# Performance work log

Measured on AMD Instinct MI355X. Metric: run time of the kernel, lower is better.

Reference implementation:

```python
import jax, jax.numpy as jnp
import numpy as np

IMG = 224
PS = 2
C_IN = 3
EMBED = 768
BATCH = 256
SLICES = IMG // 2            # 112
L = 2 * (SLICES // PS)       # 112 levels
K = IMG * PS                 # 448 gathered (a,b) pairs per level
D_IN = K * C_IN              # 1344


def _build_levels(n=IMG, slices=SLICES, ps=PS):
    """Replicates LUnraveling index construction (natural order; set() in the
    original only permutes within a level, which is equivalent up to a fixed
    permutation of weight columns for random init)."""
    a_list, b_list = [], []
    ar = np.arange(n)
    for i in range(slices // ps):
        cols = range(i * ps, (i + 1) * ps)
        # 'up' level: pairs (j, col) for j in range(n), concatenated over ps cols
        a_list.append(np.concatenate([ar for _ in cols]))
        b_list.append(np.concatenate([np.full(n, c) for c in cols]))
        # 'right' level: pairs (n - slices + col, j) for j in range(n)
        a_list.append(np.concatenate([np.full(n, n - slices + c) for c in cols]))
        b_list.append(np.concatenate([ar for _ in cols]))
    return (np.stack(a_list).astype(np.int32), np.stack(b_list).astype(np.int32))


def setup_inputs() -> dict:
    key = jax.random.key(0)
    k1, k2, k3 = jax.random.split(key, 3)
    x = jax.random.normal(k1, (BATCH, C_IN, IMG, IMG), dtype=jnp.float32)
    W = jax.random.normal(k2, (EMBED, D_IN), dtype=jnp.float32) * (1.0 / np.sqrt(D_IN))
    b = jax.random.normal(k3, (EMBED,), dtype=jnp.float32) * 0.01
    a_np, b_np = _build_levels()
    return {"x": x, "W": W, "b": b,
            "a_idx": jnp.asarray(a_np), "b_idx": jnp.asarray(b_np)}


def reference(x, W, b, a_idx, b_idx):
    B = x.shape[0]
    # gather: x[:, :, a, b] with (L,K) index arrays -> (B, C, L, K)
    g = x[:, :, a_idx, b_idx]
    # per-level flatten(1) in torch flattens (C, K) C-major -> (B, L, C*K)
    g = jnp.transpose(g, (0, 2, 1, 3)).reshape(B, L, C_IN * K)
    # shared linear projection per level token
    tokens = jnp.einsum('bld,ed->ble', g, W) + b
    return tokens  # (B, L, EMBED); norm is Identity (norm_layer=None)
```

## Files before the change

### kernel.cpp

```cpp
#include <hip/hip_runtime.h>
#include <stdint.h>


#define IMG   224
#define NLEV  112
#define CIN   3
#define DIN   1344
#define EMB   768
#define BATCH 256
#define MTOT  28672
#define NT    21

#define BM    128
#define BN    128
#define BK    64
#define LDP   72

#define AS1 __attribute__((address_space(1)))
#define AS3 __attribute__((address_space(3)))

typedef __attribute__((ext_vector_type(8))) short   short8;
typedef __attribute__((ext_vector_type(4))) float   floatx4;

__device__ __forceinline__ unsigned short f2bf(float f) {
    unsigned u = __float_as_uint(f);
    unsigned r = (u + 0x7fffu + ((u >> 16) & 1u)) >> 16;
    return (unsigned short)r;
}
__device__ __forceinline__ float bf2f(unsigned short s) {
    return __uint_as_float(((unsigned)s) << 16);
}
__device__ __forceinline__ unsigned pack2(float a, float b) {
    return (unsigned)f2bf(a) | ((unsigned)f2bf(b) << 16);
}

__global__ void detect_dtype(const unsigned short* __restrict__ W, int* flag) {
    __shared__ int s;
    if (threadIdx.x == 0) s = 0;
    __syncthreads();
    int bad = 0;
    for (int k = threadIdx.x; k < 4096; k += 256) {
        unsigned v = (unsigned)W[2 * k] & 0x7FFFu;
        if (v >= 0x4000u) bad = 1;
    }
    if (bad) atomicOr(&s, 1);
    __syncthreads();
    if (threadIdx.x == 0) *flag = s;
}

__global__ __launch_bounds__(256)
void pack_all(const void* __restrict__ Xv, const void* __restrict__ Wv,
              const void* __restrict__ Bv,
              unsigned short* __restrict__ Gc, unsigned short* __restrict__ Wb,
              float* __restrict__ Bf, int b0, int chb, int doW)
{
    __shared__ __align__(16) unsigned short lds[IMG * 128];
    __shared__ int sflag;

    const int tid = threadIdx.x;

    {
        if (tid == 0) sflag = 0;
        int bad = 0;
        const unsigned short* Wu = (const unsigned short*)Wv;
        #pragma unroll
        for (int k = tid; k < 512; k += 256) {
            unsigned v = (unsigned)Wu[2 * k] & 0x7FFFu;
            if (v >= 0x4000u) bad = 1;
        }
        __syncthreads();
        if (bad) atomicOr(&sflag, 1);
        __syncthreads();
    }
    const bool F32 = (sflag != 0);

    if (blockIdx.y == 3) {
        if (!doW) return;
        const int total = EMB * DIN / 8;
        for (int idx = blockIdx.x * 256 + tid; idx < total; idx += chb * 256) {
            if (F32) {
                const float4* s = (const float4*)((const float*)Wv + (size_t)idx * 8);
                float4 x0 = s[0], x1 = s[1];
                uint4 o;
                o.x = pack2(x0.x, x0.y); o.y = pack2(x0.z, x0.w);
                o.z = pack2(x1.x, x1.y); o.w = pack2(x1.z, x1.w);
                ((uint4*)Wb)[idx] = o;
            } else {
                ((uint4*)Wb)[idx] = ((const uint4*)Wv)[idx];
            }
        }
        if (blockIdx.x == 0) {
            for (int e = tid; e < EMB; e += 256)
                Bf[e] = F32 ? ((const float*)Bv)[e]
                            : bf2f(((const unsigned short*)Bv)[e]);
        }
        return;
    }

    const int bl = blockIdx.x;
    const int c  = blockIdx.y;
    const size_t plane = ((size_t)(b0 + bl) * CIN + c) * (size_t)(IMG * IMG);
    unsigned short* Grow = Gc + (size_t)bl * NLEV * DIN + (size_t)c * 448;

    if (F32) {
        const float* src = (const float*)Xv + plane + (size_t)NLEV * IMG;
        for (int v = tid; v < 3136; v += 256) {
            const int i  = v / 56;
            const int kk = (v - i * 56) * 8;
            const float4* s = (const float4*)(src + (size_t)v * 8);
            float4 x0 = s[0], x1 = s[1];
            uint4 o;
            o.x = pack2(x0.x, x0.y); o.y = pack2(x0.z, x0.w);
            o.z = pack2(x1.x, x1.y); o.w = pack2(x1.z, x1.w);
            *(uint4*)(Grow + (size_t)(2 * i + 1) * DIN + kk) = o;
        }
    } else {
        const unsigned short* src = (const unsigned short*)Xv + plane + (size_t)NLEV * IMG;
        for (int v = tid; v < 3136; v += 256) {
            const int i  = v / 56;
            const int kk = (v - i * 56) * 8;
            *(uint4*)(Grow + (size_t)(2 * i + 1) * DIN + kk) =
                *(const uint4*)(src + (size_t)v * 8);
        }
    }

    for (int v = tid; v < 3136; v += 256) {
        const int r  = v / 14;
        const int vv = v - r * 14;
        const int key = (r >> 3) & 15;
        uint2 o0, o1;
        if (F32) {
            const float4* s = (const float4*)((const float*)Xv + plane
                              + (size_t)r * IMG + (size_t)vv * 8);
            float4 x0 = s[0], x1 = s[1];
            o0.x = pack2(x0.x, x0.y); o0.y = pack2(x0.z, x0.w);
            o1.x = pack2(x1.x, x1.y); o1.y = pack2(x1.z, x1.w);
        } else {
            const uint2* s = (const uint2*)((const unsigned short*)Xv + plane
                              + (size_t)r * IMG + (size_t)vv * 8);
            o0 = s[0]; o1 = s[1];
        }
        *(uint2*)&lds[r * 128 + ((2 * vv)     ^ key) * 4] = o0;
        *(uint2*)&lds[r * 128 + ((2 * vv + 1) ^ key) * 4] = o1;
    }
    __syncthreads();

    for (int idx = tid; idx < 56 * 56; idx += 256) {
        const int pr   = idx / 56;
        const int j    = idx - pr * 56;
        const int half = j / 28;
        const int r0   = (j - half * 28) * 8;
        const int qb   = pr >> 1;
        const int sh   = (pr & 1) * 2;
        unsigned short h[8];
        #pragma unroll
        for (int m = 0; m < 8; m++) {
            const int r = r0 + m;
            const unsigned v = *(const unsigned*)
                &lds[r * 128 + (qb ^ ((r >> 3) & 15)) * 4 + sh];
            h[m] = half ? (unsigned short)(v >> 16) : (unsigned short)(v & 0xFFFFu);
        }
        uint4 o;
        o.x = (unsigned)h[0] | ((unsigned)h[1] << 16);
        o.y = (unsigned)h[2] | ((unsigned)h[3] << 16);
        o.z = (unsigned)h[4] | ((unsigned)h[5] << 16);
        o.w = (unsigned)h[6] | ((unsigned)h[7] << 16);
        *(uint4*)(Grow + (size_t)(2 * pr) * DIN + half * IMG + r0) = o;
    }
}

__global__ __launch_bounds__(256)
void gemm_packed(const unsigned short* __restrict__ G,
                 const unsigned short* __restrict__ Wb,
                 const float* __restrict__ Bf,
                 float* __restrict__ Out)
{
    __shared__ __align__(16) unsigned short As[2][128 * 64];
    __shared__ __align__(16) unsigned short Bs[2][128 * 64];

    const int tid  = threadIdx.x;
    const int wave = tid >> 6;
    const int lane = tid & 63;

    const int bid = blockIdx.x;
    const int nwg = gridDim.x;
    const int q = nwg >> 3, r = nwg & 7;
    const int xcd = bid & 7, s = bid >> 3;
    const int lid = (xcd < r ? xcd * (q + 1) : r * (q + 1) + (xcd - r) * q) + s;
    const int mT = lid / 6;
    const int nT = lid - mT * 6;
    const int mBase = mT * 128;
    const int nBase = nT * 128;

    const int wm   = wave >> 1, wn = wave & 1;
    const int lrow = lane & 15;
    const int kq   = (lane >> 4) << 3;
    const int swz  = (lrow & 7) << 3;

    floatx4 acc[4][4];
    #pragma unroll
    for (int i = 0; i < 4; i++)
        #pragma unroll
        for (int j = 0; j < 4; j++)
            acc[i][j] = (floatx4){0.f, 0.f, 0.f, 0.f};

    const unsigned short* gaP[4];
    const unsigned short* gbP[4];
    unsigned ldsOff[4];
    #pragma unroll
    for (int i = 0; i < 4; i++) {
        const int idx = (i * 4 + wave) * 64 + lane;
        const int row = idx >> 3, k8 = idx & 7;
        const int jc  = k8 ^ (row & 7);
        gaP[i] = G  + (size_t)(mBase + row) * DIN + jc * 8;
        gbP[i] = Wb + (size_t)(nBase + row) * DIN + jc * 8;
        ldsOff[i] = (unsigned)((i * 4 + wave) * 512);
    }

    #pragma unroll
    for (int i = 0; i < 4; i++) {
        __builtin_amdgcn_global_load_lds((const AS1 void*)(gaP[i]),
                                         (AS3 void*)(&As[0][0] + ldsOff[i]), 16, 0, 0);
        __builtin_amdgcn_global_load_lds((const AS1 void*)(gbP[i]),
                                         (AS3 void*)(&Bs[0][0] + ldsOff[i]), 16, 0, 0);
    }

    int cur = 0;
    for (int t = 0; t < NT; ++t) {
        if (t < NT - 1) {
            const int kt = (t + 1) * 64;
            #pragma unroll
            for (int i = 0; i < 4; i++) {
                __builtin_amdgcn_global_load_lds(
                    (const AS1 void*)(gaP[i] + kt),
                    (AS3 void*)(&As[cur ^ 1][0] + ldsOff[i]), 16, 0, 0);
                __builtin_amdgcn_global_load_lds(
                    (const AS1 void*)(gbP[i] + kt),
                    (AS3 void*)(&Bs[cur ^ 1][0] + ldsOff[i]), 16, 0, 0);
            }
            asm volatile("s_waitcnt vmcnt(8)" ::: "memory");
        } else {
            asm volatile("s_waitcnt vmcnt(0)" ::: "memory");
        }
        __builtin_amdgcn_s_barrier();
        __builtin_amdgcn_sched_barrier(0);

        const unsigned short* Ab = &As[cur][0];
        const unsigned short* Bb = &Bs[cur][0];
        #pragma unroll
        for (int k0 = 0; k0 < 64; k0 += 32) {
            short8 af[4], bfv[4];
            #pragma unroll
            for (int mi = 0; mi < 4; mi++)
                af[mi] = *(const short8*)&Ab[(wm * 64 + mi * 16 + lrow) * 64
                                             + ((k0 + kq) ^ swz)];
            #pragma unroll
            for (int ni = 0; ni < 4; ni++)
                bfv[ni] = *(const short8*)&Bb[(wn * 64 + ni * 16 + lrow) * 64
                                              + ((k0 + kq) ^ swz)];
            __builtin_amdgcn_s_setprio(1);
            #pragma unroll
            for (int mi = 0; mi < 4; mi++)
                #pragma unroll
                for (int ni = 0; ni < 4; ni++)
                    acc[mi][ni] = __builtin_amdgcn_mfma_f32_16x16x32_bf16(
                        af[mi], bfv[ni], acc[mi][ni], 0, 0, 0);
            __builtin_amdgcn_s_setprio(0);
        }
        __builtin_amdgcn_s_barrier();
        __builtin_amdgcn_sched_barrier(0);
        cur ^= 1;
    }

    const int quad = lane >> 4;
    #pragma unroll
    for (int ni = 0; ni < 4; ni++) {
        const int col = nBase + wn * 64 + ni * 16 + lrow;
        const float bv = Bf[col];
        #pragma unroll
        for (int mi = 0; mi < 4; mi++) {
            const int rbase = mBase + wm * 64 + mi * 16 + quad * 4;
            floatx4 a = acc[mi][ni];
            Out[(size_t)(rbase + 0) * EMB + col] = a[0] + bv;
            Out[(size_t)(rbase + 1) * EMB + col] = a[1] + bv;
            Out[(size_t)(rbase + 2) * EMB + col] = a[2] + bv;
            Out[(size_t)(rbase + 3) * EMB + col] = a[3] + bv;
        }
    }
}

template<bool F32>
__global__ __launch_bounds__(256, 2)
void lfreq_fused_gemm(const void* __restrict__ Xv,
                      const void* __restrict__ Wv,
                      const void* __restrict__ Bv,
                      const int* __restrict__ Aidx,
                      const int* __restrict__ Bidx,
                      float* __restrict__ Out,
                      const int* __restrict__ flag)
{
    if (*flag != (F32 ? 1 : 0)) return;

    __shared__ __align__(16) unsigned short As[BM][LDP];
    __shared__ __align__(16) unsigned short Bs[BN][LDP];

    const int tid   = threadIdx.x;
    const int wave  = tid >> 6;
    const int lane  = tid & 63;
    const int mBase = blockIdx.x * BM;
    const int nBase = blockIdx.y * BN;

    const int srow  = tid >> 1;
    const int shalf = tid & 1;
    const int am = mBase + srow;
    const int bb = am / NLEV;
    const int ll = am - bb * NLEV;

    floatx4 acc[4][4];
    #pragma unroll
    for (int i = 0; i < 4; i++)
        #pragma unroll
        for (int jj = 0; jj < 4; jj++)
            acc[i][jj] = (floatx4){0.f, 0.f, 0.f, 0.f};

    const int wm   = wave >> 1;
    const int wn   = wave & 1;
    const int lrow = lane & 15;
    const int kq   = (lane >> 4) << 3;

    for (int kt = 0; kt < DIN; kt += BK) {
        {
            const int koff = kt + shalf * 32;
            uint4* dst = (uint4*)&Bs[srow][shalf * 32];
            if (F32) {
                const float4* g = (const float4*)((const float*)Wv
                                + (size_t)(nBase + srow) * DIN + koff);
                #pragma unroll
                for (int q = 0; q < 4; q++) {
                    float4 v0 = g[2*q], v1 = g[2*q+1];
                    uint4 o;
                    o.x = pack2(v0.x, v0.y); o.y = pack2(v0.z, v0.w);
                    o.z = pack2(v1.x, v1.y); o.w = pack2(v1.z, v1.w);
                    dst[q] = o;
                }
            } else {
                const uint4* g = (const uint4*)((const unsigned short*)Wv
                               + (size_t)(nBase + srow) * DIN + koff);
                #pragma unroll
                for (int q = 0; q < 4; q++) dst[q] = g[q];
            }
        }
        {
            const int d0  = kt + shalf * 32;
            const int c   = (d0 >= 896) ? 2 : (d0 >= 448 ? 1 : 0);
            const int kk0 = d0 - c * 448;
            const int4* ap = (const int4*)(Aidx + ll * 448 + kk0);
            const int4* bp = (const int4*)(Bidx + ll * 448 + kk0);
            unsigned* du = (unsigned*)&As[srow][shalf * 32];
            if (F32) {
                const float* plane = (const float*)Xv
                    + (size_t)bb * (CIN * IMG * IMG) + (size_t)c * (IMG * IMG);
                #pragma unroll
                for (int q = 0; q < 8; q++) {
                    int4 av = ap[q], bv = bp[q];
                    du[2*q+0] = pack2(plane[av.x * IMG + bv.x], plane[av.y * IMG + bv.y]);
                    du[2*q+1] = pack2(plane[av.z * IMG + bv.z], plane[av.w * IMG + bv.w]);
                }
            } else {
                const unsigned short* plane = (const unsigned short*)Xv
                    + (size_t)bb * (CIN * IMG * IMG) + (size_t)c * (IMG * IMG);
                #pragma unroll
                for (int q = 0; q < 8; q++) {
                    int4 av = ap[q], bv = bp[q];
                    unsigned e0 = plane[av.x * IMG + bv.x];
                    unsigned e1 = plane[av.y * IMG + bv.y];
                    unsigned e2 = plane[av.z * IMG + bv.z];
                    unsigned e3 = plane[av.w * IMG + bv.w];
                    du[2*q+0] = e0 | (e1 << 16);
                    du[2*q+1] = e2 | (e3 << 16);
                }
            }
        }
        __syncthreads();

        #pragma unroll
        for (int k0 = 0; k0 < BK; k0 += 32) {
            short8 af[4], bfv[4];
            #pragma unroll
            for (int mi = 0; mi < 4; mi++)
                af[mi] = *(const short8*)&As[wm*64 + mi*16 + lrow][k0 + kq];
            #pragma unroll
            for (int ni = 0; ni < 4; ni++)
                bfv[ni] = *(const short8*)&Bs[wn*64 + ni*16 + lrow][k0 + kq];
            #pragma unroll
            for (int mi = 0; mi < 4; mi++)
                #pragma unroll
                for (int ni = 0; ni < 4; ni++)
                    acc[mi][ni] = __builtin_amdgcn_mfma_f32_16x16x32_bf16(
                        af[mi], bfv[ni], acc[mi][ni], 0, 0, 0);
        }
        __syncthreads();
    }

    const int quad = lane >> 4;
    #pragma unroll
    for (int ni = 0; ni < 4; ni++) {
        const int col = nBase + wn*64 + ni*16 + lrow;
        const float bv = F32 ? ((const float*)Bv)[col]
                             : bf2f(((const unsigned short*)Bv)[col]);
        #pragma unroll
        for (int mi = 0; mi < 4; mi++) {
            const int rbase = mBase + wm*64 + mi*16 + quad*4;
            floatx4 a = acc[mi][ni];
            Out[(size_t)(rbase+0)*EMB + col] = a[0] + bv;
            Out[(size_t)(rbase+1)*EMB + col] = a[1] + bv;
            Out[(size_t)(rbase+2)*EMB + col] = a[2] + bv;
            Out[(size_t)(rbase+3)*EMB + col] = a[3] + bv;
        }
    }
}

extern "C" void kernel_launch(void* const* d_in, const int* in_sizes, int n_in,
                              void* d_out, int out_size, void* d_ws, size_t ws_size,
                              hipStream_t stream) {
    const void* X    = d_in[0];
    const void* Wt   = d_in[1];
    const void* Bias = d_in[2];
    const int*  Ai   = (const int*)d_in[3];
    const int*  Bi   = (const int*)d_in[4];
    float* Out = (float*)d_out;

    char* ws  = (char*)d_ws;
    int* flag = (int*)ws;

    float* Bf          = (float*)(ws + 256);
    unsigned short* Wb = (unsigned short*)(ws + 4096);
    const size_t gOff  = 4096 + (size_t)EMB * DIN * 2;
    unsigned short* Gc = (unsigned short*)(ws + gOff);

    int CHB = 0;
    const int cand[6] = {256, 128, 64, 32, 16, 8};
    for (int t = 0; t < 6; t++) {
        if (gOff + (size_t)cand[t] * NLEV * DIN * 2 <= ws_size) { CHB = cand[t]; break; }
    }

    if (CHB == 0) {
        detect_dtype<<<dim3(1), dim3(256), 0, stream>>>((const unsigned short*)Wt, flag);
        dim3 grid(MTOT / BM, EMB / BN);
        lfreq_fused_gemm<false><<<grid, dim3(256), 0, stream>>>(X, Wt, Bias, Ai, Bi, Out, flag);
        lfreq_fused_gemm<true ><<<grid, dim3(256), 0, stream>>>(X, Wt, Bias, Ai, Bi, Out, flag);
        return;
    }

    for (int b0 = 0; b0 < BATCH; b0 += CHB) {
        dim3 pgrid(CHB, 4);
        pack_all<<<pgrid, dim3(256), 0, stream>>>(X, Wt, Bias, Gc, Wb, Bf,
                                                  b0, CHB, b0 == 0 ? 1 : 0);
        dim3 ggrid(CHB * NLEV / 128 * 6);
        gemm_packed<<<ggrid, dim3(256), 0, stream>>>(Gc, Wb, Bf,
                                                     Out + (size_t)b0 * NLEV * EMB);
    }
}
```

Before: 334.0 us.

## Enlarge GEMM tile to 256x128 and read odd levels directly from input in bf16 mode

The GEMM goes to 512 threads with a 256-row M tile, so each block reuses its loaded W tile across twice as many rows. When the inputs are already bf16, the GEMM now loads the odd 'right' levels straight from the raw image and W straight from the raw weights. This removes the copy passes in the pack kernel for that case. The pack kernel writes the dtype flag for the GEMM to read, and the CHB=8 chunk option is dropped. In the default fp32 path the main effect is the larger tile, which raises register and LDS pressure per block and halves the grid size.

```diff
diff --git a/kernel.cpp b/kernel.cpp
--- a/kernel.cpp
+++ b/kernel.cpp
@@ -10,6 +10,8 @@
 #define BATCH 256
 #define MTOT  28672
 #define NT    21
+#define GBM   256
+#define GBN   128
 
 #define BM    128
 #define BN    128
@@ -52,7 +54,8 @@
 void pack_all(const void* __restrict__ Xv, const void* __restrict__ Wv,
               const void* __restrict__ Bv,
               unsigned short* __restrict__ Gc, unsigned short* __restrict__ Wb,
-              float* __restrict__ Bf, int b0, int chb, int doW)
+              float* __restrict__ Bf, int* __restrict__ flagOut,
+              int b0, int chb, int doW)
 {
     __shared__ __align__(16) unsigned short lds[IMG * 128];
     __shared__ int sflag;
@@ -74,19 +77,20 @@
     }
     const bool F32 = (sflag != 0);
 
+    if (blockIdx.x == 0 && blockIdx.y == 0 && tid == 0)
+        *flagOut = F32 ? 1 : 0;
+
     if (blockIdx.y == 3) {
         if (!doW) return;
-        const int total = EMB * DIN / 8;
-        for (int idx = blockIdx.x * 256 + tid; idx < total; idx += chb * 256) {
-            if (F32) {
+        if (F32) {
+            const int total = EMB * DIN / 8;
+            for (int idx = blockIdx.x * 256 + tid; idx < total; idx += chb * 256) {
                 const float4* s = (const float4*)((const float*)Wv + (size_t)idx * 8);
                 float4 x0 = s[0], x1 = s[1];
                 uint4 o;
                 o.x = pack2(x0.x, x0.y); o.y = pack2(x0.z, x0.w);
                 o.z = pack2(x1.x, x1.y); o.w = pack2(x1.z, x1.w);
                 ((uint4*)Wb)[idx] = o;
-            } else {
-                ((uint4*)Wb)[idx] = ((const uint4*)Wv)[idx];
             }
         }
         if (blockIdx.x == 0) {
@@ -113,14 +117,6 @@
             o.x = pack2(x0.x, x0.y); o.y = pack2(x0.z, x0.w);
             o.z = pack2(x1.x, x1.y); o.w = pack2(x1.z, x1.w);
             *(uint4*)(Grow + (size_t)(2 * i + 1) * DIN + kk) = o;
-        }
-    } else {
-        const unsigned short* src = (const unsigned short*)Xv + plane + (size_t)NLEV * IMG;
-        for (int v = tid; v < 3136; v += 256) {
-            const int i  = v / 56;
-            const int kk = (v - i * 56) * 8;
-            *(uint4*)(Grow + (size_t)(2 * i + 1) * DIN + kk) =
-                *(const uint4*)(src + (size_t)v * 8);
         }
     }
 
@@ -169,18 +165,23 @@
     }
 }
 
-__global__ __launch_bounds__(256)
+__global__ __launch_bounds__(512)
 void gemm_packed(const unsigned short* __restrict__ G,
+                 const unsigned short* __restrict__ Xu,
+                 const unsigned short* __restrict__ Wraw,
                  const unsigned short* __restrict__ Wb,
                  const float* __restrict__ Bf,
-                 float* __restrict__ Out)
+                 float* __restrict__ Out,
+                 const int* __restrict__ flag,
+                 int b0)
 {
-    __shared__ __align__(16) unsigned short As[2][128 * 64];
-    __shared__ __align__(16) unsigned short Bs[2][128 * 64];
+    __shared__ __align__(16) unsigned short As[2][GBM * 64];
+    __shared__ __align__(16) unsigned short Bs[2][GBN * 64];
 
     const int tid  = threadIdx.x;
     const int wave = tid >> 6;
     const int lane = tid & 63;
+    const bool useX = (*flag == 0);
 
     const int bid = blockIdx.x;
     const int nwg = gridDim.x;
@@ -189,14 +190,16 @@
     const int lid = (xcd < r ? xcd * (q + 1) : r * (q + 1) + (xcd - r) * q) + s;
     const int mT = lid / 6;
     const int nT = lid - mT * 6;
-    const int mBase = mT * 128;
-    const int nBase = nT * 128;
+    const int mBase = mT * GBM;
+    const int nBase = nT * GBN;
 
     const int wm   = wave >> 1, wn = wave & 1;
     const int lrow = lane & 15;
     const int kq   = (lane >> 4) << 3;
     const int swz  = (lrow & 7) << 3;
 
+    const unsigned short* Wsrc = useX ? Wraw : Wb;
+
     floatx4 acc[4][4];
     #pragma unroll
     for (int i = 0; i < 4; i++)
@@ -204,41 +207,63 @@
         for (int j = 0; j < 4; j++)
             acc[i][j] = (floatx4){0.f, 0.f, 0.f, 0.f};
 
-    const unsigned short* gaP[4];
-    const unsigned short* gbP[4];
-    unsigned ldsOff[4];
+    const unsigned short* aP[4];
+    int aExtra[4];
+    unsigned aOff[4];
     #pragma unroll
     for (int i = 0; i < 4; i++) {
-        const int idx = (i * 4 + wave) * 64 + lane;
+        const int idx = (i * 8 + wave) * 64 + lane;
         const int row = idx >> 3, k8 = idx & 7;
         const int jc  = k8 ^ (row & 7);
-        gaP[i] = G  + (size_t)(mBase + row) * DIN + jc * 8;
-        gbP[i] = Wb + (size_t)(nBase + row) * DIN + jc * 8;
-        ldsOff[i] = (unsigned)((i * 4 + wave) * 512);
-    }
-
-    #pragma unroll
-    for (int i = 0; i < 4; i++) {
-        __builtin_amdgcn_global_load_lds((const AS1 void*)(gaP[i]),
-                                         (AS3 void*)(&As[0][0] + ldsOff[i]), 16, 0, 0);
-        __builtin_amdgcn_global_load_lds((const AS1 void*)(gbP[i]),
-                                         (AS3 void*)(&Bs[0][0] + ldsOff[i]), 16, 0, 0);
-    }
+        const int m   = mBase + row;
+        const int b   = m / NLEV;
+        const int l   = m - b * NLEV;
+        if ((l & 1) && useX) {
+            aP[i] = Xu + (size_t)(b0 + b) * (CIN * IMG * IMG)
+                       + (size_t)(111 + l) * IMG + jc * 8;
+            aExtra[i] = 49728;
+        } else {
+            aP[i] = G + (size_t)m * DIN + jc * 8;
+            aExtra[i] = 0;
+        }
+        aOff[i] = (unsigned)((i * 8 + wave) * 512);
+    }
+    const unsigned short* bP[2];
+    unsigned bOff[2];
+    #pragma unroll
+    for (int i = 0; i < 2; i++) {
+        const int idx = (i * 8 + wave) * 64 + lane;
+        const int row = idx >> 3, k8 = idx & 7;
+        const int jc  = k8 ^ (row & 7);
+        bP[i] = Wsrc + (size_t)(nBase + row) * DIN + jc * 8;
+        bOff[i] = (unsigned)((i * 8 + wave) * 512);
+    }
+
+    #pragma unroll
+    for (int i = 0; i < 4; i++)
+        __builtin_amdgcn_global_load_lds((const AS1 void*)(aP[i]),
+                                         (AS3 void*)(&As[0][0] + aOff[i]), 16, 0, 0);
+    #pragma unroll
+    for (int i = 0; i < 2; i++)
+        __builtin_amdgcn_global_load_lds((const AS1 void*)(bP[i]),
+                                         (AS3 void*)(&Bs[0][0] + bOff[i]), 16, 0, 0);
 
     int cur = 0;
     for (int t = 0; t < NT; ++t) {
         if (t < NT - 1) {
             const int kt = (t + 1) * 64;
-            #pragma unroll
-            for (int i = 0; i < 4; i++) {
+            const int c  = kt / 448;
+            #pragma unroll
+            for (int i = 0; i < 4; i++)
                 __builtin_amdgcn_global_load_lds(
-                    (const AS1 void*)(gaP[i] + kt),
-                    (AS3 void*)(&As[cur ^ 1][0] + ldsOff[i]), 16, 0, 0);
+                    (const AS1 void*)(aP[i] + kt + c * aExtra[i]),
+                    (AS3 void*)(&As[cur ^ 1][0] + aOff[i]), 16, 0, 0);
+            #pragma unroll
+            for (int i = 0; i < 2; i++)
                 __builtin_amdgcn_global_load_lds(
-                    (const AS1 void*)(gbP[i] + kt),
-                    (AS3 void*)(&Bs[cur ^ 1][0] + ldsOff[i]), 16, 0, 0);
-            }
-            asm volatile("s_waitcnt vmcnt(8)" ::: "memory");
+                    (const AS1 void*)(bP[i] + kt),
+                    (AS3 void*)(&Bs[cur ^ 1][0] + bOff[i]), 16, 0, 0);
+            asm volatile("s_waitcnt vmcnt(6)" ::: "memory");
         } else {
             asm volatile("s_waitcnt vmcnt(0)" ::: "memory");
         }
@@ -439,8 +464,8 @@
     unsigned short* Gc = (unsigned short*)(ws + gOff);
 
     int CHB = 0;
-    const int cand[6] = {256, 128, 64, 32, 16, 8};
-    for (int t = 0; t < 6; t++) {
+    const int cand[5] = {256, 128, 64, 32, 16};
+    for (int t = 0; t < 5; t++) {
         if (gOff + (size_t)cand[t] * NLEV * DIN * 2 <= ws_size) { CHB = cand[t]; break; }
     }
 
@@ -454,10 +479,11 @@
 
     for (int b0 = 0; b0 < BATCH; b0 += CHB) {
         dim3 pgrid(CHB, 4);
-        pack_all<<<pgrid, dim3(256), 0, stream>>>(X, Wt, Bias, Gc, Wb, Bf,
+        pack_all<<<pgrid, dim3(256), 0, stream>>>(X, Wt, Bias, Gc, Wb, Bf, flag,
                                                   b0, CHB, b0 == 0 ? 1 : 0);
-        dim3 ggrid(CHB * NLEV / 128 * 6);
-        gemm_packed<<<ggrid, dim3(256), 0, stream>>>(Gc, Wb, Bf,
-                                                     Out + (size_t)b0 * NLEV * EMB);
-    }
-}
+        dim3 ggrid(CHB * NLEV / GBM * 6);
+        gemm_packed<<<ggrid, dim3(512), 0, stream>>>(
+            Gc, (const unsigned short*)X, (const unsigned short*)Wt, Wb, Bf,
+            Out + (size_t)b0 * NLEV * EMB, flag, b0);
+    }
+}
```

New measurement: 354.8 us. +6.2%, slower.
